# Kernel optimization log

Hardware: AMD Instinct MI355X
Metric: run time of the kernel (lower is better)

## Reference

```python
import jax, jax.numpy as jnp
import numpy as np

N_NODES = 50000
N_EDGES = 800000
D = 64
H = 128

def _mlp(x, W1, b1, W2, b2):
    return jax.nn.relu(x @ W1 + b1) @ W2 + b2

def setup_inputs() -> dict:
    key = jax.random.key(0)
    ks = jax.random.split(key, 16)
    s = 0.05
    inp = {
        'nf': jax.random.normal(ks[0], (N_NODES, D), jnp.float32),
        'ef': jax.random.normal(ks[1], (N_EDGES, D), jnp.float32),
        'u': jax.random.normal(ks[2], (1, D), jnp.float32),
        'eW1': jax.random.normal(ks[3], (4 * D, H), jnp.float32) * s,
        'eb1': jnp.zeros((H,), jnp.float32),
        'eW2': jax.random.normal(ks[4], (H, D), jnp.float32) * s,
        'eb2': jnp.zeros((D,), jnp.float32),
        'nW1': jax.random.normal(ks[5], (3 * D, H), jnp.float32) * s,
        'nb1': jnp.zeros((H,), jnp.float32),
        'nW2': jax.random.normal(ks[6], (H, D), jnp.float32) * s,
        'nb2': jnp.zeros((D,), jnp.float32),
        'gW1': jax.random.normal(ks[7], (3 * D, H), jnp.float32) * s,
        'gb1': jnp.zeros((H,), jnp.float32),
        'gW2': jax.random.normal(ks[8], (H, D), jnp.float32) * s,
        'gb2': jnp.zeros((D,), jnp.float32),
        'src': jax.random.randint(ks[9], (N_EDGES,), 0, N_NODES, jnp.int32),
        'dst': jax.random.randint(ks[10], (N_EDGES,), 0, N_NODES, jnp.int32),
    }
    return inp

def reference(nf, ef, u, eW1, eb1, eW2, eb2, nW1, nb1, nW2, nb2, gW1, gb1, gW2, gb2, src, dst):
    E = ef.shape[0]
    N = nf.shape[0]
    u_e = jnp.broadcast_to(u, (E, u.shape[-1]))  # repeat_interleave over edges (single graph)
    # edge update: concat(sender, receiver, ef, u) -> MLP
    em_in = jnp.concatenate([nf[src], nf[dst], ef, u_e], axis=-1)  # [E, 4D]
    updated_ef = _mlp(em_in, eW1, eb1, eW2, eb2)  # [E, D]
    # mean aggregation of messages per destination node (copy_e + mean)
    deg = jax.ops.segment_sum(jnp.ones((E,), nf.dtype), dst, num_segments=N)
    agg_m = jax.ops.segment_sum(updated_ef, dst, num_segments=N) / jnp.maximum(deg, 1.0)[:, None]
    # node update: concat(agg_m, nf, u) -> MLP
    u_n = jnp.broadcast_to(u, (N, u.shape[-1]))
    nm_in = jnp.concatenate([agg_m, nf, u_n], axis=-1)  # [N, 3D]
    updated_nf = _mlp(nm_in, nW1, nb1, nW2, nb2)  # [N, D]
    # global update: mean readouts of updated node/edge features
    node_readout = jnp.mean(updated_nf, axis=0, keepdims=True)
    edge_readout = jnp.mean(updated_ef, axis=0, keepdims=True)
    gm_in = jnp.concatenate([node_readout, edge_readout, u], axis=-1)  # [1, 3D]
    updated_u = _mlp(gm_in, gW1, gb1, gW2, gb2)
    # residual
    return (updated_nf + nf, updated_ef + ef, updated_u + u)
```

## Files before the change

### kernel.cpp

```cpp
#include <hip/hip_runtime.h>
#include <hip/hip_bf16.h>

typedef __bf16 bf16x8 __attribute__((ext_vector_type(8)));
typedef __bf16 bf16x4 __attribute__((ext_vector_type(4)));
typedef float  f32x4  __attribute__((ext_vector_type(4)));

#define SWZ(row, byte) ((byte) ^ (((row) & 15) << 4))

__global__ __launch_bounds__(256) void prep_all(
    const float* __restrict__ nf, __bf16* __restrict__ nfb, int nElem,
    const float* __restrict__ eW1, const float* __restrict__ eW2,
    const float* __restrict__ nW1, const float* __restrict__ nW2,
    const float* __restrict__ u,
    __bf16* __restrict__ w1e_f, __bf16* __restrict__ w2e_f,
    __bf16* __restrict__ w1n_f, __bf16* __restrict__ w2n_f,
    __bf16* __restrict__ ub,
    const int* __restrict__ dst, int* __restrict__ degi, int E,
    int B_NF, int B_W)
{
    int b = blockIdx.x;
    if (b < B_NF) {
        int i = (b * 256 + threadIdx.x) * 4;
        if (i < nElem) {
            float4 v = *reinterpret_cast<const float4*>(nf + i);
            bf16x4 o;
            o[0] = (__bf16)v.x; o[1] = (__bf16)v.y; o[2] = (__bf16)v.z; o[3] = (__bf16)v.w;
            *reinterpret_cast<bf16x4*>(nfb + i) = o;
        }
    } else if (b < B_NF + B_W) {
        int p = (b - B_NF) * 256 + threadIdx.x;
        if (p < 32768) {
            int i = p & 7, l = (p >> 3) & 63, f = p >> 9;
            int kk = f >> 3, nt = f & 7, lo = l & 15, hi = l >> 4;
            w1e_f[p] = (__bf16)eW1[(kk * 32 + hi * 8 + i) * 128 + nt * 16 + lo];
        } else if (p < 40960) {
            int j = p - 32768;
            int i = j & 7, l = (j >> 3) & 63, g = j >> 9;
            int kk = g >> 2, nt = g & 3, lo = l & 15, hi = l >> 4;
            w2e_f[j] = (__bf16)eW2[(kk * 32 + hi * 8 + i) * 64 + nt * 16 + lo];
        } else if (p < 65536) {
            int j = p - 40960;
            int i = j & 7, l = (j >> 3) & 63, f = j >> 9;
            int kk = f >> 3, nt = f & 7, lo = l & 15, hi = l >> 4;
            w1n_f[j] = (__bf16)nW1[(kk * 32 + hi * 8 + i) * 128 + nt * 16 + lo];
        } else if (p < 73728) {
            int j = p - 65536;
            int i = j & 7, l = (j >> 3) & 63, g = j >> 9;
            int kk = g >> 2, nt = g & 3, lo = l & 15, hi = l >> 4;
            w2n_f[j] = (__bf16)nW2[(kk * 32 + hi * 8 + i) * 64 + nt * 16 + lo];
        } else if (p < 73792) {
            ub[p - 73728] = (__bf16)u[p - 73728];
        }
    } else {
        int e = (b - B_NF - B_W) * 256 + threadIdx.x;
        if (e < E) atomicAdd(&degi[dst[e]], 1);
    }
}

__global__ __launch_bounds__(256) void scan_local(const int* __restrict__ degi,
                                                  int* __restrict__ offs,
                                                  int* __restrict__ bsum, int N) {
    __shared__ int sm[256];
    const int t = threadIdx.x;
    int i = blockIdx.x * 256 + t;
    int v = (i < N) ? degi[i] : 0;
    sm[t] = v;
    __syncthreads();
    for (int d = 1; d < 256; d <<= 1) {
        int a = (t >= d) ? sm[t - d] : 0;
        __syncthreads();
        sm[t] += a;
        __syncthreads();
    }
    if (i < N) offs[i] = sm[t] - v;
    if (t == 255) bsum[blockIdx.x] = sm[t];
}

__global__ __launch_bounds__(256) void scan_blocks(const int* __restrict__ bsum,
                                                   int* __restrict__ bofs, int nb) {
    __shared__ int sm[256];
    const int t = threadIdx.x;
    int v = (t < nb) ? bsum[t] : 0;
    sm[t] = v;
    __syncthreads();
    for (int d = 1; d < 256; d <<= 1) {
        int a = (t >= d) ? sm[t - d] : 0;
        __syncthreads();
        sm[t] += a;
        __syncthreads();
    }
    if (t < nb) bofs[t] = sm[t] - v;
}

__global__ __launch_bounds__(256) void scan_add(int* __restrict__ offs,
                                                const int* __restrict__ bofs, int N) {
    int i = blockIdx.x * 256 + threadIdx.x;
    if (i < N) offs[i] += bofs[blockIdx.x];
}

__global__ __launch_bounds__(256) void fill_kernel(const int* __restrict__ dst,
                                                   const int* __restrict__ off,
                                                   int* __restrict__ cursor,
                                                   int* __restrict__ eidx, int E) {
    int e = blockIdx.x * 256 + threadIdx.x;
    if (e < E) {
        int d = dst[e];
        int slot = atomicAdd(&cursor[d], 1);
        eidx[off[d] + slot] = e;
    }
}

__global__ __launch_bounds__(512, 4) void edge_mfma(
    const float* __restrict__ ef,
    const __bf16* __restrict__ nfb, const __bf16* __restrict__ ub,
    const bf16x8* __restrict__ w1f, const bf16x8* __restrict__ w2f,
    const float* __restrict__ b1, const float* __restrict__ b2,
    const int* __restrict__ src, const int* __restrict__ dst,
    const int* __restrict__ eidx,
    float* __restrict__ out_e, float* __restrict__ agg,
    int E)
{
    __shared__ alignas(16) char lds[49152];
    const int tid = threadIdx.x;
    const int w = tid >> 6, l = tid & 63;
    const int lo = l & 15, hi = l >> 4;
    const long wb = (long)blockIdx.x * 128 + w * 16;

    long jL = wb + lo;
    const bool vL = (jL < E);
    const int eA = vL ? eidx[jL] : 0;
    const int srcA = src[eA];
    const int dstA = vL ? dst[eA] : -1;

    bf16x8 afr[8];
#pragma unroll
    for (int kk = 0; kk < 8; ++kk) {
        const int koff = (kk & 1) * 32 + hi * 8;
        const int sec = kk >> 1;
        if (sec == 0) {
            afr[kk] = *(const bf16x8*)(nfb + (size_t)srcA * 64 + koff);
        } else if (sec == 1) {
            int dg = (dstA >= 0) ? dstA : 0;
            afr[kk] = *(const bf16x8*)(nfb + (size_t)dg * 64 + koff);
        } else if (sec == 2) {
            const float* p = ef + (size_t)eA * 64 + koff;
            float4 v0 = *(const float4*)p;
            float4 v1 = *(const float4*)(p + 4);
            bf16x8 t;
            t[0] = (__bf16)v0.x; t[1] = (__bf16)v0.y; t[2] = (__bf16)v0.z; t[3] = (__bf16)v0.w;
            t[4] = (__bf16)v1.x; t[5] = (__bf16)v1.y; t[6] = (__bf16)v1.z; t[7] = (__bf16)v1.w;
            afr[kk] = t;
        } else {
            afr[kk] = *(const bf16x8*)(ub + koff);
        }
    }

    int erA[4];
#pragma unroll
    for (int r = 0; r < 4; ++r)
        erA[r] = __shfl(eA, hi * 4 + r);
    float resv[4][4];
#pragma unroll
    for (int r = 0; r < 4; ++r)
#pragma unroll
        for (int nt = 0; nt < 4; ++nt)
            resv[r][nt] = ef[(size_t)erA[r] * 64 + nt * 16 + lo];

    float b1v[8];
#pragma unroll
    for (int nt = 0; nt < 8; ++nt) b1v[nt] = b1[nt * 16 + lo];
    float b2v[4];
#pragma unroll
    for (int nt = 0; nt < 4; ++nt) b2v[nt] = b2[nt * 16 + lo];

#pragma unroll
    for (int p = tid; p < 2048; p += 512)
        *(bf16x8*)(lds + p * 16) = w1f[p];
#pragma unroll
    for (int p = tid; p < 1024; p += 512)
        *(bf16x8*)(lds + 32768 + p * 16) = w2f[p];
    __syncthreads();

    f32x4 acc1[8] = {};
#pragma unroll
    for (int kk = 0; kk < 4; ++kk)
#pragma unroll
        for (int nt = 0; nt < 8; ++nt) {
            bf16x8 bfr = *(const bf16x8*)(lds + ((kk * 8 + nt) * 64 + l) * 16);
            acc1[nt] = __builtin_amdgcn_mfma_f32_16x16x32_bf16(afr[kk], bfr, acc1[nt], 0, 0, 0);
        }
    __syncthreads();

#pragma unroll
    for (int p = tid; p < 2048; p += 512)
        *(bf16x8*)(lds + p * 16) = w1f[2048 + p];
    __syncthreads();

#pragma unroll
    for (int kk = 4; kk < 8; ++kk)
#pragma unroll
        for (int nt = 0; nt < 8; ++nt) {
            bf16x8 bfr = *(const bf16x8*)(lds + (((kk - 4) * 8 + nt) * 64 + l) * 16);
            acc1[nt] = __builtin_amdgcn_mfma_f32_16x16x32_bf16(afr[kk], bfr, acc1[nt], 0, 0, 0);
        }
    __syncthreads();

    char* hp = lds + w * 4096;
#pragma unroll
    for (int nt = 0; nt < 8; ++nt) {
        int col = nt * 16 + lo;
#pragma unroll
        for (int r = 0; r < 4; ++r) {
            int row = hi * 4 + r;
            float hv = fmaxf(acc1[nt][r] + b1v[nt], 0.0f);
            *(__bf16*)(hp + SWZ(row, row * 256 + col * 2)) = (__bf16)hv;
        }
    }

    f32x4 acc2[4] = {};
#pragma unroll
    for (int kk = 0; kk < 4; ++kk) {
        int kb = (kk * 32 + hi * 8) * 2;
        bf16x8 a0 = *(const bf16x8*)(hp + SWZ(lo, lo * 256 + kb));
#pragma unroll
        for (int nt = 0; nt < 4; ++nt) {
            bf16x8 bfr = *(const bf16x8*)(lds + 32768 + ((kk * 4 + nt) * 64 + l) * 16);
            acc2[nt] = __builtin_amdgcn_mfma_f32_16x16x32_bf16(a0, bfr, acc2[nt], 0, 0, 0);
        }
    }

#pragma unroll
    for (int nt = 0; nt < 4; ++nt)
#pragma unroll
        for (int r = 0; r < 4; ++r)
            acc2[nt][r] += b2v[nt];

#pragma unroll
    for (int r = 0; r < 4; ++r) {
        int row = hi * 4 + r;
        if (wb + row >= E) continue;
#pragma unroll
        for (int nt = 0; nt < 4; ++nt)
            out_e[(size_t)erA[r] * 64 + nt * 16 + lo] = acc2[nt][r] + resv[r][nt];
    }

    int dn = __shfl(dstA, (l + 1) & 63);
    unsigned long long bal = __ballot(dstA != dn);
    unsigned mm = ((unsigned)bal & 0x7FFFu) | 0x8000u;
    int startRow = 0;
    while (mm) {
        int endRow = __ffs(mm);
        int d = __shfl(dstA, startRow);
        if (d >= 0) {
            float s0 = 0.f, s1 = 0.f, s2 = 0.f, s3 = 0.f;
#pragma unroll
            for (int r = 0; r < 4; ++r) {
                int row = hi * 4 + r;
                if (row >= startRow && row < endRow) {
                    s0 += acc2[0][r];
                    s1 += acc2[1][r];
                    s2 += acc2[2][r];
                    s3 += acc2[3][r];
                }
            }
            s0 += __shfl_xor(s0, 16); s0 += __shfl_xor(s0, 32);
            s1 += __shfl_xor(s1, 16); s1 += __shfl_xor(s1, 32);
            s2 += __shfl_xor(s2, 16); s2 += __shfl_xor(s2, 32);
            s3 += __shfl_xor(s3, 16); s3 += __shfl_xor(s3, 32);
            if (l < 16) {
                float* ap = agg + (size_t)d * 64;
                atomicAdd(ap + l,      s0);
                atomicAdd(ap + 16 + l, s1);
                atomicAdd(ap + 32 + l, s2);
                atomicAdd(ap + 48 + l, s3);
            }
        }
        startRow = endRow;
        mm &= mm - 1;
    }
}

__global__ __launch_bounds__(512, 4) void node_mfma(
    const float* __restrict__ nf,
    const __bf16* __restrict__ nfb, const __bf16* __restrict__ ub,
    const float* __restrict__ agg, const int* __restrict__ degi,
    const bf16x8* __restrict__ w1f, const bf16x8* __restrict__ w2f,
    const float* __restrict__ b1, const float* __restrict__ b2,
    float* __restrict__ out_n, float* __restrict__ nsum_part,
    int N)
{
    __shared__ alignas(16) char lds[49152];
    const int tid = threadIdx.x;
    const int w = tid >> 6, l = tid & 63;
    const int lo = l & 15, hi = l >> 4;
    const long nb = (long)blockIdx.x * 128 + w * 16;

    long gnL = nb + lo;
    const int gnA = (gnL < N) ? (int)gnL : 0;
    const float inv = 1.0f / fmaxf((float)degi[gnA], 1.0f);

    bf16x8 afr[6];
#pragma unroll
    for (int kk = 0; kk < 6; ++kk) {
        const int koff = (kk & 1) * 32 + hi * 8;
        const int sec = kk >> 1;
        if (sec == 0) {
            const float* p = agg + (size_t)gnA * 64 + koff;
            float4 v0 = *(const float4*)p;
            float4 v1 = *(const float4*)(p + 4);
            bf16x8 t;
            t[0] = (__bf16)(v0.x * inv); t[1] = (__bf16)(v0.y * inv);
            t[2] = (__bf16)(v0.z * inv); t[3] = (__bf16)(v0.w * inv);
            t[4] = (__bf16)(v1.x * inv); t[5] = (__bf16)(v1.y * inv);
            t[6] = (__bf16)(v1.z * inv); t[7] = (__bf16)(v1.w * inv);
            afr[kk] = t;
        } else if (sec == 1) {
            afr[kk] = *(const bf16x8*)(nfb + (size_t)gnA * 64 + koff);
        } else {
            afr[kk] = *(const bf16x8*)(ub + koff);
        }
    }

    float b1v[8];
#pragma unroll
    for (int nt = 0; nt < 8; ++nt) b1v[nt] = b1[nt * 16 + lo];
    float b2v[4];
#pragma unroll
    for (int nt = 0; nt < 4; ++nt) b2v[nt] = b2[nt * 16 + lo];

#pragma unroll
    for (int p = tid; p < 1536; p += 512)
        *(bf16x8*)(lds + p * 16) = w1f[p];
#pragma unroll
    for (int p = tid; p < 1024; p += 512)
        *(bf16x8*)(lds + 32768 + p * 16) = w2f[p];
    __syncthreads();

    f32x4 acc1[8] = {};
#pragma unroll
    for (int kk = 0; kk < 3; ++kk)
#pragma unroll
        for (int nt = 0; nt < 8; ++nt) {
            bf16x8 bfr = *(const bf16x8*)(lds + ((kk * 8 + nt) * 64 + l) * 16);
            acc1[nt] = __builtin_amdgcn_mfma_f32_16x16x32_bf16(afr[kk], bfr, acc1[nt], 0, 0, 0);
        }
    __syncthreads();

#pragma unroll
    for (int p = tid; p < 1536; p += 512)
        *(bf16x8*)(lds + p * 16) = w1f[1536 + p];
    __syncthreads();

#pragma unroll
    for (int kk = 3; kk < 6; ++kk)
#pragma unroll
        for (int nt = 0; nt < 8; ++nt) {
            bf16x8 bfr = *(const bf16x8*)(lds + (((kk - 3) * 8 + nt) * 64 + l) * 16);
            acc1[nt] = __builtin_amdgcn_mfma_f32_16x16x32_bf16(afr[kk], bfr, acc1[nt], 0, 0, 0);
        }
    __syncthreads();

    char* hp = lds + w * 4096;
#pragma unroll
    for (int nt = 0; nt < 8; ++nt) {
        int col = nt * 16 + lo;
#pragma unroll
        for (int r = 0; r < 4; ++r) {
            int row = hi * 4 + r;
            float hv = fmaxf(acc1[nt][r] + b1v[nt], 0.0f);
            *(__bf16*)(hp + SWZ(row, row * 256 + col * 2)) = (__bf16)hv;
        }
    }

    f32x4 acc2[4] = {};
#pragma unroll
    for (int kk = 0; kk < 4; ++kk) {
        int kb = (kk * 32 + hi * 8) * 2;
        bf16x8 a0 = *(const bf16x8*)(hp + SWZ(lo, lo * 256 + kb));
#pragma unroll
        for (int nt = 0; nt < 4; ++nt) {
            bf16x8 bfr = *(const bf16x8*)(lds + 32768 + ((kk * 4 + nt) * 64 + l) * 16);
            acc2[nt] = __builtin_amdgcn_mfma_f32_16x16x32_bf16(a0, bfr, acc2[nt], 0, 0, 0);
        }
    }

    float vsum[4] = {0.f, 0.f, 0.f, 0.f};
#pragma unroll
    for (int r = 0; r < 4; ++r) {
        long gn = nb + hi * 4 + r;
        if (gn >= N) continue;
        int gni = (int)gn;
#pragma unroll
        for (int nt = 0; nt < 4; ++nt) {
            int col = nt * 16 + lo;
            float msg = acc2[nt][r] + b2v[nt];
            out_n[(size_t)gni * 64 + col] = msg + nf[(size_t)gni * 64 + col];
            vsum[nt] += msg;
        }
    }
#pragma unroll
    for (int nt = 0; nt < 4; ++nt) {
        float v = vsum[nt];
        v += __shfl_xor(v, 16);
        v += __shfl_xor(v, 32);
        if (l < 16) nsum_part[((size_t)blockIdx.x * 8 + w) * 64 + nt * 16 + l] = v;
    }
}

__global__ __launch_bounds__(256) void reduce_two(
    const float* __restrict__ aggIn, float* __restrict__ edge_sum, int RA, int NBA,
    const float* __restrict__ nsumIn, float* __restrict__ node_sum, int RB, int NBB)
{
    const float* in; float* out; int R, rb, nb;
    if ((int)blockIdx.x < NBA) { in = aggIn;  out = edge_sum; R = RA; rb = blockIdx.x;       nb = NBA; }
    else                       { in = nsumIn; out = node_sum; R = RB; rb = blockIdx.x - NBA; nb = NBB; }
    int col = threadIdx.x & 63;
    float s = 0.f;
    for (int r = rb * 4 + (threadIdx.x >> 6); r < R; r += nb * 4)
        s += in[(size_t)r * 64 + col];
    __shared__ float sm[256];
    sm[threadIdx.x] = s;
    __syncthreads();
    if (threadIdx.x < 64) {
        float v = sm[threadIdx.x] + sm[threadIdx.x + 64] + sm[threadIdx.x + 128] + sm[threadIdx.x + 192];
        atomicAdd(&out[threadIdx.x], v);
    }
}

__global__ __launch_bounds__(128) void global_kernel(
    const float* __restrict__ u,
    const float* __restrict__ W1, const float* __restrict__ b1,
    const float* __restrict__ W2, const float* __restrict__ b2,
    const float* __restrict__ node_sum, const float* __restrict__ edge_sum,
    float* __restrict__ out_u, int N, int E)
{
    __shared__ float gm[192];
    __shared__ float h[128];
    int tid = threadIdx.x;
    if (tid < 64) {
        gm[tid]       = node_sum[tid] / (float)N;
        gm[64 + tid]  = edge_sum[tid] / (float)E;
        gm[128 + tid] = u[tid];
    }
    __syncthreads();
    float a = b1[tid];
    for (int k = 0; k < 192; ++k) a = fmaf(gm[k], W1[k * 128 + tid], a);
    h[tid] = fmaxf(a, 0.f);
    __syncthreads();
    if (tid < 64) {
        float o = b2[tid];
        for (int k = 0; k < 128; ++k) o = fmaf(h[k], W2[k * 64 + tid], o);
        out_u[tid] = o + u[tid];
    }
}

extern "C" void kernel_launch(void* const* d_in, const int* in_sizes, int n_in,
                              void* d_out, int out_size, void* d_ws, size_t ws_size,
                              hipStream_t stream) {
    const float* nf  = (const float*)d_in[0];
    const float* ef  = (const float*)d_in[1];
    const float* u   = (const float*)d_in[2];
    const float* eW1 = (const float*)d_in[3];
    const float* eb1 = (const float*)d_in[4];
    const float* eW2 = (const float*)d_in[5];
    const float* eb2 = (const float*)d_in[6];
    const float* nW1 = (const float*)d_in[7];
    const float* nb1 = (const float*)d_in[8];
    const float* nW2 = (const float*)d_in[9];
    const float* nb2 = (const float*)d_in[10];
    const float* gW1 = (const float*)d_in[11];
    const float* gb1 = (const float*)d_in[12];
    const float* gW2 = (const float*)d_in[13];
    const float* gb2 = (const float*)d_in[14];
    const int*   src = (const int*)d_in[15];
    const int*   dst = (const int*)d_in[16];

    const int N = in_sizes[0] / 64;
    const int E = in_sizes[1] / 64;
    const int EDGE_BLOCKS = (E + 127) / 128;
    const int NODE_BLOCKS = (N + 127) / 128;
    const int SCAN_NB = (N + 255) / 256;

    char* ws = (char*)d_ws;
    size_t off_b = 0;
    auto alloc = [&](size_t bytes) { size_t c = off_b; off_b += (bytes + 255) & ~(size_t)255; return c; };

    int*    degi     = (int*)(ws + alloc((size_t)N * 4));
    int*    cursor   = (int*)(ws + alloc((size_t)N * 4));
    float*  edge_sum = (float*)(ws + alloc(256));
    float*  node_sum = (float*)(ws + alloc(256));
    float*  agg      = (float*)(ws + alloc((size_t)N * 64 * 4));
    size_t  zero_bytes = off_b;
    int*    offs     = (int*)(ws + alloc((size_t)N * 4));
    int*    bsum     = (int*)(ws + alloc((size_t)SCAN_NB * 4));
    int*    bofs     = (int*)(ws + alloc((size_t)SCAN_NB * 4));
    int*    eidx     = (int*)(ws + alloc((size_t)E * 4));
    float*  nsum_part= (float*)(ws + alloc((size_t)NODE_BLOCKS * 8 * 64 * 4));
    __bf16* nfb   = (__bf16*)(ws + alloc((size_t)N * 64 * 2));
    __bf16* ub    = (__bf16*)(ws + alloc(256));
    __bf16* w1e_f = (__bf16*)(ws + alloc(32768 * 2));
    __bf16* w2e_f = (__bf16*)(ws + alloc(8192 * 2));
    __bf16* w1n_f = (__bf16*)(ws + alloc(24576 * 2));
    __bf16* w2n_f = (__bf16*)(ws + alloc(8192 * 2));

    float* out_n = (float*)d_out;
    float* out_e = out_n + (size_t)N * 64;
    float* out_u = out_e + (size_t)E * 64;

    const int B_NF = (N * 16 + 255) / 256;
    const int B_W  = (73792 + 255) / 256;
    const int B_H  = (E + 255) / 256;

    hipMemsetAsync(d_ws, 0, zero_bytes, stream);
    prep_all<<<B_NF + B_W + B_H, 256, 0, stream>>>(
        nf, nfb, N * 64, eW1, eW2, nW1, nW2, u,
        w1e_f, w2e_f, w1n_f, w2n_f, ub, dst, degi, E, B_NF, B_W);
    scan_local<<<SCAN_NB, 256, 0, stream>>>(degi, offs, bsum, N);
    scan_blocks<<<1, 256, 0, stream>>>(bsum, bofs, SCAN_NB);
    scan_add<<<SCAN_NB, 256, 0, stream>>>(offs, bofs, N);
    fill_kernel<<<(E + 255) / 256, 256, 0, stream>>>(dst, offs, cursor, eidx, E);
    edge_mfma<<<EDGE_BLOCKS, 512, 0, stream>>>(
        ef, nfb, ub, (const bf16x8*)w1e_f, (const bf16x8*)w2e_f, eb1, eb2,
        src, dst, eidx, out_e, agg, E);
    node_mfma<<<NODE_BLOCKS, 512, 0, stream>>>(
        nf, nfb, ub, agg, degi, (const bf16x8*)w1n_f, (const bf16x8*)w2n_f,
        nb1, nb2, out_n, nsum_part, N);
    reduce_two<<<128 + 16, 256, 0, stream>>>(
        agg, edge_sum, N, 128, nsum_part, node_sum, NODE_BLOCKS * 8, 16);
    global_kernel<<<1, 128, 0, stream>>>(
        u, gW1, gb1, gW2, gb2, node_sum, edge_sum, out_u, N, E);
}
```

Measured before the change: 366.8 us.

## Make edge MLP kernel persistent with resident weights and prefetched gathers

The edge kernel becomes persistent: a fixed grid of 256 blocks of 768 threads loops over 192-edge tiles. The full first- and second-layer weights are loaded into 128KB of dynamic LDS once per block instead of being reloaded in two halves for every tile. Each iteration prefetches the next tile's node/edge gathers and index loads while the current tile's MFMAs run. The scan_add kernel is removed by adding the block offset inside fill_kernel. The cost is lower occupancy (one large block per CU) and more live registers, and it depends on the large dynamic LDS allocation being accepted.

After: 413.7 us. +12.8%, slower.

```diff
diff --git a/kernel.cpp b/kernel.cpp
--- a/kernel.cpp
+++ b/kernel.cpp
@@ -92,25 +92,63 @@
     if (t < nb) bofs[t] = sm[t] - v;
 }
 
-__global__ __launch_bounds__(256) void scan_add(int* __restrict__ offs,
-                                                const int* __restrict__ bofs, int N) {
-    int i = blockIdx.x * 256 + threadIdx.x;
-    if (i < N) offs[i] += bofs[blockIdx.x];
-}
-
 __global__ __launch_bounds__(256) void fill_kernel(const int* __restrict__ dst,
-                                                   const int* __restrict__ off,
+                                                   const int* __restrict__ offs,
+                                                   const int* __restrict__ bofs,
                                                    int* __restrict__ cursor,
                                                    int* __restrict__ eidx, int E) {
     int e = blockIdx.x * 256 + threadIdx.x;
     if (e < E) {
         int d = dst[e];
         int slot = atomicAdd(&cursor[d], 1);
-        eidx[off[d] + slot] = e;
-    }
-}
-
-__global__ __launch_bounds__(512, 4) void edge_mfma(
+        eidx[offs[d] + bofs[d >> 8] + slot] = e;
+    }
+}
+
+#define LOAD_IDX(BB, EAV, SAV, DAV)                                            \
+    {                                                                          \
+        long jL_ = (long)(BB) * 192 + w * 16 + lo;                             \
+        bool v_ = ((BB) < (long)NB) && (jL_ < (long)E);                        \
+        EAV = v_ ? eidx[jL_] : 0;                                              \
+        SAV = src[EAV];                                                        \
+        DAV = v_ ? dst[EAV] : -1;                                              \
+    }
+
+#define GATHERS(SAV, DAV, EAV, RV, ER)                                         \
+    {                                                                          \
+        _Pragma("unroll")                                                      \
+        for (int kk = 0; kk < 8; ++kk) {                                       \
+            const int koff_ = (kk & 1) * 32 + hi * 8;                          \
+            const int sec_ = kk >> 1;                                          \
+            if (sec_ == 0) {                                                   \
+                afr[kk] = *(const bf16x8*)(nfb + (size_t)(SAV) * 64 + koff_);  \
+            } else if (sec_ == 1) {                                            \
+                int dg_ = ((DAV) >= 0) ? (DAV) : 0;                            \
+                afr[kk] = *(const bf16x8*)(nfb + (size_t)dg_ * 64 + koff_);    \
+            } else if (sec_ == 2) {                                            \
+                const float* p_ = ef + (size_t)(EAV) * 64 + koff_;             \
+                float4 v0_ = *(const float4*)p_;                               \
+                float4 v1_ = *(const float4*)(p_ + 4);                         \
+                bf16x8 t_;                                                     \
+                t_[0] = (__bf16)v0_.x; t_[1] = (__bf16)v0_.y;                  \
+                t_[2] = (__bf16)v0_.z; t_[3] = (__bf16)v0_.w;                  \
+                t_[4] = (__bf16)v1_.x; t_[5] = (__bf16)v1_.y;                  \
+                t_[6] = (__bf16)v1_.z; t_[7] = (__bf16)v1_.w;                  \
+                afr[kk] = t_;                                                  \
+            } else {                                                           \
+                afr[kk] = *(const bf16x8*)(ub + koff_);                        \
+            }                                                                  \
+        }                                                                      \
+        _Pragma("unroll")                                                      \
+        for (int r = 0; r < 4; ++r) ER[r] = __shfl((EAV), hi * 4 + r);         \
+        _Pragma("unroll")                                                      \
+        for (int r = 0; r < 4; ++r)                                            \
+            _Pragma("unroll")                                                  \
+            for (int nt = 0; nt < 4; ++nt)                                     \
+                RV[r][nt] = ef[(size_t)ER[r] * 64 + nt * 16 + lo];             \
+    }
+
+__global__ __launch_bounds__(768, 3) void edge_mfma(
     const float* __restrict__ ef,
     const __bf16* __restrict__ nfb, const __bf16* __restrict__ ub,
     const bf16x8* __restrict__ w1f, const bf16x8* __restrict__ w2f,
@@ -118,165 +156,138 @@
     const int* __restrict__ src, const int* __restrict__ dst,
     const int* __restrict__ eidx,
     float* __restrict__ out_e, float* __restrict__ agg,
-    int E)
+    int E, int NB, int iters)
 {
-    __shared__ alignas(16) char lds[49152];
+    extern __shared__ char lds[];
     const int tid = threadIdx.x;
     const int w = tid >> 6, l = tid & 63;
     const int lo = l & 15, hi = l >> 4;
-    const long wb = (long)blockIdx.x * 128 + w * 16;
-
-    long jL = wb + lo;
-    const bool vL = (jL < E);
-    const int eA = vL ? eidx[jL] : 0;
-    const int srcA = src[eA];
-    const int dstA = vL ? dst[eA] : -1;
+    char* hp = lds + 81920 + w * 4096;
+
+    for (int p = tid; p < 4096; p += 768)
+        *(bf16x8*)(lds + p * 16) = w1f[p];
+    for (int p = tid; p < 1024; p += 768)
+        *(bf16x8*)(lds + 65536 + p * 16) = w2f[p];
+
+    float b1v[8], b2v[4];
+#pragma unroll
+    for (int nt = 0; nt < 8; ++nt) b1v[nt] = b1[nt * 16 + lo];
+#pragma unroll
+    for (int nt = 0; nt < 4; ++nt) b2v[nt] = b2[nt * 16 + lo];
 
     bf16x8 afr[8];
-#pragma unroll
-    for (int kk = 0; kk < 8; ++kk) {
-        const int koff = (kk & 1) * 32 + hi * 8;
-        const int sec = kk >> 1;
-        if (sec == 0) {
-            afr[kk] = *(const bf16x8*)(nfb + (size_t)srcA * 64 + koff);
-        } else if (sec == 1) {
-            int dg = (dstA >= 0) ? dstA : 0;
-            afr[kk] = *(const bf16x8*)(nfb + (size_t)dg * 64 + koff);
-        } else if (sec == 2) {
-            const float* p = ef + (size_t)eA * 64 + koff;
-            float4 v0 = *(const float4*)p;
-            float4 v1 = *(const float4*)(p + 4);
-            bf16x8 t;
-            t[0] = (__bf16)v0.x; t[1] = (__bf16)v0.y; t[2] = (__bf16)v0.z; t[3] = (__bf16)v0.w;
-            t[4] = (__bf16)v1.x; t[5] = (__bf16)v1.y; t[6] = (__bf16)v1.z; t[7] = (__bf16)v1.w;
-            afr[kk] = t;
-        } else {
-            afr[kk] = *(const bf16x8*)(ub + koff);
-        }
-    }
-
-    int erA[4];
+    int eAn, srcAn, dstAn;
+    int dstC, erC[4], erN[4];
+    float resvC[4][4], resvN[4][4];
+
+    LOAD_IDX((long)blockIdx.x, eAn, srcAn, dstAn);
+    GATHERS(srcAn, dstAn, eAn, resvN, erN);
+    dstC = dstAn;
+#pragma unroll
+    for (int r = 0; r < 4; ++r) erC[r] = erN[r];
 #pragma unroll
     for (int r = 0; r < 4; ++r)
-        erA[r] = __shfl(eA, hi * 4 + r);
-    float resv[4][4];
-#pragma unroll
-    for (int r = 0; r < 4; ++r)
-#pragma unroll
-        for (int nt = 0; nt < 4; ++nt)
-            resv[r][nt] = ef[(size_t)erA[r] * 64 + nt * 16 + lo];
-
-    float b1v[8];
-#pragma unroll
-    for (int nt = 0; nt < 8; ++nt) b1v[nt] = b1[nt * 16 + lo];
-    float b2v[4];
-#pragma unroll
-    for (int nt = 0; nt < 4; ++nt) b2v[nt] = b2[nt * 16 + lo];
-
-#pragma unroll
-    for (int p = tid; p < 2048; p += 512)
-        *(bf16x8*)(lds + p * 16) = w1f[p];
-#pragma unroll
-    for (int p = tid; p < 1024; p += 512)
-        *(bf16x8*)(lds + 32768 + p * 16) = w2f[p];
-    __syncthreads();
-
-    f32x4 acc1[8] = {};
-#pragma unroll
-    for (int kk = 0; kk < 4; ++kk)
+#pragma unroll
+        for (int nt = 0; nt < 4; ++nt) resvC[r][nt] = resvN[r][nt];
+    LOAD_IDX((long)blockIdx.x + 256, eAn, srcAn, dstAn);
+
+    __syncthreads();
+
+    for (int k = 0; k < iters; ++k) {
+        f32x4 acc1[8] = {};
+#pragma unroll
+        for (int kk = 0; kk < 8; ++kk)
+#pragma unroll
+            for (int nt = 0; nt < 8; ++nt) {
+                bf16x8 bfr = *(const bf16x8*)(lds + ((kk * 8 + nt) * 64 + l) * 16);
+                acc1[nt] = __builtin_amdgcn_mfma_f32_16x16x32_bf16(afr[kk], bfr, acc1[nt], 0, 0, 0);
+            }
+
+        GATHERS(srcAn, dstAn, eAn, resvN, erN);
+
+        int eAf, srcAf, dstAf;
+        LOAD_IDX((long)blockIdx.x + (long)(k + 2) * 256, eAf, srcAf, dstAf);
+
 #pragma unroll
         for (int nt = 0; nt < 8; ++nt) {
-            bf16x8 bfr = *(const bf16x8*)(lds + ((kk * 8 + nt) * 64 + l) * 16);
-            acc1[nt] = __builtin_amdgcn_mfma_f32_16x16x32_bf16(afr[kk], bfr, acc1[nt], 0, 0, 0);
-        }
-    __syncthreads();
-
-#pragma unroll
-    for (int p = tid; p < 2048; p += 512)
-        *(bf16x8*)(lds + p * 16) = w1f[2048 + p];
-    __syncthreads();
-
-#pragma unroll
-    for (int kk = 4; kk < 8; ++kk)
-#pragma unroll
-        for (int nt = 0; nt < 8; ++nt) {
-            bf16x8 bfr = *(const bf16x8*)(lds + (((kk - 4) * 8 + nt) * 64 + l) * 16);
-            acc1[nt] = __builtin_amdgcn_mfma_f32_16x16x32_bf16(afr[kk], bfr, acc1[nt], 0, 0, 0);
-        }
-    __syncthreads();
-
-    char* hp = lds + w * 4096;
-#pragma unroll
-    for (int nt = 0; nt < 8; ++nt) {
-        int col = nt * 16 + lo;
-#pragma unroll
-        for (int r = 0; r < 4; ++r) {
-            int row = hi * 4 + r;
-            float hv = fmaxf(acc1[nt][r] + b1v[nt], 0.0f);
-            *(__bf16*)(hp + SWZ(row, row * 256 + col * 2)) = (__bf16)hv;
-        }
-    }
-
-    f32x4 acc2[4] = {};
-#pragma unroll
-    for (int kk = 0; kk < 4; ++kk) {
-        int kb = (kk * 32 + hi * 8) * 2;
-        bf16x8 a0 = *(const bf16x8*)(hp + SWZ(lo, lo * 256 + kb));
-#pragma unroll
-        for (int nt = 0; nt < 4; ++nt) {
-            bf16x8 bfr = *(const bf16x8*)(lds + 32768 + ((kk * 4 + nt) * 64 + l) * 16);
-            acc2[nt] = __builtin_amdgcn_mfma_f32_16x16x32_bf16(a0, bfr, acc2[nt], 0, 0, 0);
-        }
-    }
-
-#pragma unroll
-    for (int nt = 0; nt < 4; ++nt)
-#pragma unroll
-        for (int r = 0; r < 4; ++r)
-            acc2[nt][r] += b2v[nt];
-
-#pragma unroll
-    for (int r = 0; r < 4; ++r) {
-        int row = hi * 4 + r;
-        if (wb + row >= E) continue;
-#pragma unroll
-        for (int nt = 0; nt < 4; ++nt)
-            out_e[(size_t)erA[r] * 64 + nt * 16 + lo] = acc2[nt][r] + resv[r][nt];
-    }
-
-    int dn = __shfl(dstA, (l + 1) & 63);
-    unsigned long long bal = __ballot(dstA != dn);
-    unsigned mm = ((unsigned)bal & 0x7FFFu) | 0x8000u;
-    int startRow = 0;
-    while (mm) {
-        int endRow = __ffs(mm);
-        int d = __shfl(dstA, startRow);
-        if (d >= 0) {
-            float s0 = 0.f, s1 = 0.f, s2 = 0.f, s3 = 0.f;
+            int col = nt * 16 + lo;
 #pragma unroll
             for (int r = 0; r < 4; ++r) {
                 int row = hi * 4 + r;
-                if (row >= startRow && row < endRow) {
-                    s0 += acc2[0][r];
-                    s1 += acc2[1][r];
-                    s2 += acc2[2][r];
-                    s3 += acc2[3][r];
+                float hv = fmaxf(acc1[nt][r] + b1v[nt], 0.0f);
+                *(__bf16*)(hp + SWZ(row, row * 256 + col * 2)) = (__bf16)hv;
+            }
+        }
+
+        f32x4 acc2[4] = {};
+#pragma unroll
+        for (int kk = 0; kk < 4; ++kk) {
+            int kb = (kk * 32 + hi * 8) * 2;
+            bf16x8 a0 = *(const bf16x8*)(hp + SWZ(lo, lo * 256 + kb));
+#pragma unroll
+            for (int nt = 0; nt < 4; ++nt) {
+                bf16x8 bfr = *(const bf16x8*)(lds + 65536 + ((kk * 4 + nt) * 64 + l) * 16);
+                acc2[nt] = __builtin_amdgcn_mfma_f32_16x16x32_bf16(a0, bfr, acc2[nt], 0, 0, 0);
+            }
+        }
+#pragma unroll
+        for (int nt = 0; nt < 4; ++nt)
+#pragma unroll
+            for (int r = 0; r < 4; ++r)
+                acc2[nt][r] += b2v[nt];
+
+        long wb = ((long)blockIdx.x + (long)k * 256) * 192 + w * 16;
+#pragma unroll
+        for (int r = 0; r < 4; ++r) {
+            if (wb + hi * 4 + r >= E) continue;
+#pragma unroll
+            for (int nt = 0; nt < 4; ++nt)
+                out_e[(size_t)erC[r] * 64 + nt * 16 + lo] = acc2[nt][r] + resvC[r][nt];
+        }
+
+        int dn = __shfl(dstC, (l + 1) & 63);
+        unsigned long long bal = __ballot(dstC != dn);
+        unsigned mm = ((unsigned)bal & 0x7FFFu) | 0x8000u;
+        int startRow = 0;
+        while (mm) {
+            int endRow = __ffs(mm);
+            int d = __shfl(dstC, startRow);
+            if (d >= 0) {
+                float s0 = 0.f, s1 = 0.f, s2 = 0.f, s3 = 0.f;
+#pragma unroll
+                for (int r = 0; r < 4; ++r) {
+                    int row = hi * 4 + r;
+                    if (row >= startRow && row < endRow) {
+                        s0 += acc2[0][r];
+                        s1 += acc2[1][r];
+                        s2 += acc2[2][r];
+                        s3 += acc2[3][r];
+                    }
+                }
+                s0 += __shfl_xor(s0, 16); s0 += __shfl_xor(s0, 32);
+                s1 += __shfl_xor(s1, 16); s1 += __shfl_xor(s1, 32);
+                s2 += __shfl_xor(s2, 16); s2 += __shfl_xor(s2, 32);
+                s3 += __shfl_xor(s3, 16); s3 += __shfl_xor(s3, 32);
+                if (l < 16) {
+                    float* ap = agg + (size_t)d * 64;
+                    atomicAdd(ap + l,      s0);
+                    atomicAdd(ap + 16 + l, s1);
+                    atomicAdd(ap + 32 + l, s2);
+                    atomicAdd(ap + 48 + l, s3);
                 }
             }
-            s0 += __shfl_xor(s0, 16); s0 += __shfl_xor(s0, 32);
-            s1 += __shfl_xor(s1, 16); s1 += __shfl_xor(s1, 32);
-            s2 += __shfl_xor(s2, 16); s2 += __shfl_xor(s2, 32);
-            s3 += __shfl_xor(s3, 16); s3 += __shfl_xor(s3, 32);
-            if (l < 16) {
-                float* ap = agg + (size_t)d * 64;
-                atomicAdd(ap + l,      s0);
-                atomicAdd(ap + 16 + l, s1);
-                atomicAdd(ap + 32 + l, s2);
-                atomicAdd(ap + 48 + l, s3);
-            }
-        }
-        startRow = endRow;
-        mm &= mm - 1;
+            startRow = endRow;
+            mm &= mm - 1;
+        }
+
+        dstC = dstAn;
+#pragma unroll
+        for (int r = 0; r < 4; ++r) erC[r] = erN[r];
+#pragma unroll
+        for (int r = 0; r < 4; ++r)
+#pragma unroll
+            for (int nt = 0; nt < 4; ++nt) resvC[r][nt] = resvN[r][nt];
+        eAn = eAf; srcAn = srcAf; dstAn = dstAf;
     }
 }
 
@@ -477,9 +488,10 @@
 
     const int N = in_sizes[0] / 64;
     const int E = in_sizes[1] / 64;
-    const int EDGE_BLOCKS = (E + 127) / 128;
     const int NODE_BLOCKS = (N + 127) / 128;
     const int SCAN_NB = (N + 255) / 256;
+    const int NB_EDGE = (E + 191) / 192;
+    const int EDGE_ITERS = (NB_EDGE + 255) / 256;
 
     char* ws = (char*)d_ws;
     size_t off_b = 0;
@@ -517,11 +529,10 @@
         w1e_f, w2e_f, w1n_f, w2n_f, ub, dst, degi, E, B_NF, B_W);
     scan_local<<<SCAN_NB, 256, 0, stream>>>(degi, offs, bsum, N);
     scan_blocks<<<1, 256, 0, stream>>>(bsum, bofs, SCAN_NB);
-    scan_add<<<SCAN_NB, 256, 0, stream>>>(offs, bofs, N);
-    fill_kernel<<<(E + 255) / 256, 256, 0, stream>>>(dst, offs, cursor, eidx, E);
-    edge_mfma<<<EDGE_BLOCKS, 512, 0, stream>>>(
+    fill_kernel<<<(E + 255) / 256, 256, 0, stream>>>(dst, offs, bofs, cursor, eidx, E);
+    edge_mfma<<<256, 768, 131072, stream>>>(
         ef, nfb, ub, (const bf16x8*)w1e_f, (const bf16x8*)w2e_f, eb1, eb2,
-        src, dst, eidx, out_e, agg, E);
+        src, dst, eidx, out_e, agg, E, NB_EDGE, EDGE_ITERS);
     node_mfma<<<NODE_BLOCKS, 512, 0, stream>>>(
         nf, nfb, ub, agg, degi, (const bf16x8*)w1n_f, (const bf16x8*)w2n_f,
         nb1, nb2, out_n, nsum_part, N);
```
